# Performance work log

Hardware: AMD Instinct MI355X
Metric: run time of the kernel (lower is better)

The kernel has to match this reference:

```python
import jax, jax.numpy as jnp
import numpy as np

B, T, D, H = 512, 512, 256, 512

def setup_inputs() -> dict:
    key = jax.random.key(0)
    ks = jax.random.split(key, 7)
    s_ih = 1.0 / np.sqrt(H)
    return {
        "x": jax.random.normal(ks[0], (B, T, D), dtype=jnp.float32),
        "W_ih": jax.random.normal(ks[1], (4 * H, D), dtype=jnp.float32) * s_ih,
        "W_hh": jax.random.normal(ks[2], (4 * H, H), dtype=jnp.float32) * s_ih,
        "b_ih": jax.random.normal(ks[3], (4 * H,), dtype=jnp.float32) * s_ih,
        "b_hh": jax.random.normal(ks[4], (4 * H,), dtype=jnp.float32) * s_ih,
        "W_fc": jax.random.normal(ks[5], (1, H), dtype=jnp.float32) * s_ih,
        "b_fc": jax.random.normal(ks[6], (1,), dtype=jnp.float32) * s_ih,
    }

def reference(x, W_ih, W_hh, b_ih, b_hh, W_fc, b_fc):
    # Precompute input projections for all steps: [T, B, 4H]
    xg = jnp.einsum('btd,gd->tbg', x, W_ih) + b_ih + b_hh

    def step(carry, xg_t):
        h, c = carry
        gates = xg_t + h @ W_hh.T  # [B, 4H]
        i, f, g, o = jnp.split(gates, 4, axis=-1)  # torch LSTMCell gate order
        i = jax.nn.sigmoid(i)
        f = jax.nn.sigmoid(f)
        g = jnp.tanh(g)
        o = jax.nn.sigmoid(o)
        c = f * c + i * g
        h = o * jnp.tanh(c)
        return (h, c), None

    h0 = jnp.zeros((x.shape[0], W_hh.shape[1]), dtype=x.dtype)
    (h, _), _ = jax.lax.scan(step, (h0, h0), xg)
    # dropout in eval mode is identity
    return jax.nn.sigmoid(h @ W_fc.T + b_fc)  # [B, 1]
```

## Files before the change

### kernel.cpp

```cpp
#include <hip/hip_runtime.h>

typedef _Float16 f16;
typedef _Float16 f16x8 __attribute__((ext_vector_type(8)));
typedef float f32x4 __attribute__((ext_vector_type(4)));
typedef unsigned int u32;
typedef u32 u32x4 __attribute__((ext_vector_type(4)));
typedef unsigned long long u64;

#define TT 512
#define BB 512
#define DD 256
#define HH 512

#define WPACK_BYTES (32*4*24*64*8*2)
#define HBUF_OFF    (WPACK_BYTES)
#define HQ_SLOT     (BB*HH/4)
#define HBUF_BYTES  (4*BB*HH*2)

__device__ __forceinline__ float sigf(float v) {
    return __frcp_rn(1.0f + __expf(-v));
}
__device__ __forceinline__ float tanh_fast(float v) {
    float e = __expf(2.0f * fminf(v, 15.0f));
    return 1.0f - 2.0f * __frcp_rn(e + 1.0f);
}

__global__ void pack_w(const float* __restrict__ W_ih,
                       const float* __restrict__ W_hh,
                       f16* __restrict__ Wp) {
    int tid = blockIdx.x * 256 + threadIdx.x;
    if (tid >= 32*4*24*64) return;
    int lane = tid & 63;
    int rest = tid >> 6;
    int ks   = rest % 24;
    int t3   = rest / 24;
    int nt   = t3 & 3;
    int ji   = t3 >> 2;
    int g  = nt*512 + ji*16 + (lane & 15);
    int k0 = ks*32 + ((lane >> 4) & 3)*8;
    const float* src = (k0 < 256) ? (W_ih + (size_t)g*DD + k0)
                                  : (W_hh + (size_t)g*HH + (k0 - 256));
    f16x8 v;
    #pragma unroll
    for (int j = 0; j < 8; ++j) v[j] = (f16)src[j];
    *(f16x8*)(Wp + (size_t)tid*8) = v;
}

#define LDH16_SC1(A, p) asm volatile(                                  \
    "global_load_dwordx4 %0, %16, off sc1\n\t"                         \
    "global_load_dwordx4 %1, %16, off offset:64 sc1\n\t"               \
    "global_load_dwordx4 %2, %16, off offset:128 sc1\n\t"              \
    "global_load_dwordx4 %3, %16, off offset:192 sc1\n\t"              \
    "global_load_dwordx4 %4, %16, off offset:256 sc1\n\t"              \
    "global_load_dwordx4 %5, %16, off offset:320 sc1\n\t"              \
    "global_load_dwordx4 %6, %16, off offset:384 sc1\n\t"              \
    "global_load_dwordx4 %7, %16, off offset:448 sc1\n\t"              \
    "global_load_dwordx4 %8, %16, off offset:512 sc1\n\t"              \
    "global_load_dwordx4 %9, %16, off offset:576 sc1\n\t"              \
    "global_load_dwordx4 %10, %16, off offset:640 sc1\n\t"             \
    "global_load_dwordx4 %11, %16, off offset:704 sc1\n\t"             \
    "global_load_dwordx4 %12, %16, off offset:768 sc1\n\t"             \
    "global_load_dwordx4 %13, %16, off offset:832 sc1\n\t"             \
    "global_load_dwordx4 %14, %16, off offset:896 sc1\n\t"             \
    "global_load_dwordx4 %15, %16, off offset:960 sc1\n\t"             \
    "s_waitcnt vmcnt(0)"                                               \
    : "=&v"((A)[0]), "=&v"((A)[1]), "=&v"((A)[2]), "=&v"((A)[3]),      \
      "=&v"((A)[4]), "=&v"((A)[5]), "=&v"((A)[6]), "=&v"((A)[7]),      \
      "=&v"((A)[8]), "=&v"((A)[9]), "=&v"((A)[10]), "=&v"((A)[11]),    \
      "=&v"((A)[12]), "=&v"((A)[13]), "=&v"((A)[14]), "=&v"((A)[15])   \
    : "v"(p) : "memory")

#define LDH256_SC1(A, p) asm volatile(                                 \
    "global_load_dwordx4 %0, %16, off sc1\n\t"                         \
    "global_load_dwordx4 %1, %16, off offset:16 sc1\n\t"               \
    "global_load_dwordx4 %2, %16, off offset:32 sc1\n\t"               \
    "global_load_dwordx4 %3, %16, off offset:48 sc1\n\t"               \
    "global_load_dwordx4 %4, %16, off offset:64 sc1\n\t"               \
    "global_load_dwordx4 %5, %16, off offset:80 sc1\n\t"               \
    "global_load_dwordx4 %6, %16, off offset:96 sc1\n\t"               \
    "global_load_dwordx4 %7, %16, off offset:112 sc1\n\t"              \
    "global_load_dwordx4 %8, %16, off offset:128 sc1\n\t"              \
    "global_load_dwordx4 %9, %16, off offset:144 sc1\n\t"              \
    "global_load_dwordx4 %10, %16, off offset:160 sc1\n\t"             \
    "global_load_dwordx4 %11, %16, off offset:176 sc1\n\t"             \
    "global_load_dwordx4 %12, %16, off offset:192 sc1\n\t"             \
    "global_load_dwordx4 %13, %16, off offset:208 sc1\n\t"             \
    "global_load_dwordx4 %14, %16, off offset:224 sc1\n\t"             \
    "global_load_dwordx4 %15, %16, off offset:240 sc1\n\t"             \
    "s_waitcnt vmcnt(0)"                                               \
    : "=&v"((A)[0]), "=&v"((A)[1]), "=&v"((A)[2]), "=&v"((A)[3]),      \
      "=&v"((A)[4]), "=&v"((A)[5]), "=&v"((A)[6]), "=&v"((A)[7]),      \
      "=&v"((A)[8]), "=&v"((A)[9]), "=&v"((A)[10]), "=&v"((A)[11]),    \
      "=&v"((A)[12]), "=&v"((A)[13]), "=&v"((A)[14]), "=&v"((A)[15])   \
    : "v"(p) : "memory")

__device__ __forceinline__ bool chunk_ok(const f16x8& c) {
    u32x4 t = __builtin_bit_cast(u32x4, c);
    return ((t.y >> 16) != 0xFFFFu) && ((t.w >> 16) != 0xFFFFu);
}

__launch_bounds__(256, 1)
__global__ void lstm_fused(const float* __restrict__ x,
                           const float* __restrict__ b_ih,
                           const float* __restrict__ b_hh,
                           const float* __restrict__ W_fc,
                           const float* __restrict__ b_fc,
                           const f16* __restrict__ Wp,
                           f16* __restrict__ hbuf,
                           float* __restrict__ out) {
    extern __shared__ char smem[];
    f16x8* Wlds = (f16x8*)smem;

    const int tid  = threadIdx.x;
    const int lane = tid & 63;
    const int w    = tid >> 6;
    const int bi   = blockIdx.x & 7;
    const int ji   = blockIdx.x >> 3;

    {
        const f16x8* src = (const f16x8*)Wp + (size_t)ji * (4*24*64);
        for (int i = tid; i < 4*24*64; i += 256) Wlds[i] = src[i];
    }

    const int uq = (lane >> 4) * 4;
    float bias[4][4];
    #pragma unroll
    for (int nt = 0; nt < 4; ++nt)
        #pragma unroll
        for (int r = 0; r < 4; ++r)
            bias[nt][r] = b_ih[nt*512 + ji*16 + uq + r] + b_hh[nt*512 + ji*16 + uq + r];
    __syncthreads();

    const int batch  = bi*64 + w*16 + (lane & 15);
    const int koff   = (lane >> 4) * 8;
    const float* xrow = x + (size_t)batch * TT * DD + koff;
    u64* hq = (u64*)hbuf;
    const int hrow_q = (batch * HH + koff) >> 2;
    const int hoff_q = (batch * HH + ji*16 + uq) >> 2;

    float c[4] = {0.f, 0.f, 0.f, 0.f};
    f32x4 acc[4];

    {
        float4 xa[8], xb[8];
        #pragma unroll
        for (int ks = 0; ks < 8; ++ks) {
            xa[ks] = *(const float4*)(xrow + ks*32);
            xb[ks] = *(const float4*)(xrow + ks*32 + 4);
        }
        #pragma unroll
        for (int nt = 0; nt < 4; ++nt)
            acc[nt] = (f32x4){bias[nt][0], bias[nt][1], bias[nt][2], bias[nt][3]};
        #pragma unroll
        for (int ks = 0; ks < 8; ++ks) {
            f16x8 a;
            a[0]=(f16)xa[ks].x; a[1]=(f16)xa[ks].y; a[2]=(f16)xa[ks].z; a[3]=(f16)xa[ks].w;
            a[4]=(f16)xb[ks].x; a[5]=(f16)xb[ks].y; a[6]=(f16)xb[ks].z; a[7]=(f16)xb[ks].w;
            #pragma unroll
            for (int nt = 0; nt < 4; ++nt)
                acc[nt] = __builtin_amdgcn_mfma_f32_16x16x32_f16(
                    Wlds[(nt*24 + ks)*64 + lane], a, acc[nt], 0, 0, 0);
        }
    }

    for (int s = 0; s < TT; ++s) {
        if (s > 0) {
            const u64* hb = hq + (size_t)(s & 3) * HQ_SLOT + hrow_q;
            f16x8 Ah[16];
            for (;;) {
                LDH16_SC1(Ah, hb);
                bool ok = true;
                #pragma unroll
                for (int ks = 0; ks < 16; ++ks) ok = ok && chunk_ok(Ah[ks]);
                if (__all(ok)) break;
                __builtin_amdgcn_s_sleep(2);
            }
            if (s + 3 <= TT)
                __hip_atomic_store(hq + (size_t)((s + 3) & 3) * HQ_SLOT + hoff_q,
                                   0xFFFFFFFFFFFFFFFFull, __ATOMIC_RELAXED,
                                   __HIP_MEMORY_SCOPE_AGENT);
            #pragma unroll
            for (int ks = 0; ks < 16; ++ks)
                #pragma unroll
                for (int nt = 0; nt < 4; ++nt)
                    acc[nt] = __builtin_amdgcn_mfma_f32_16x16x32_f16(
                        Wlds[(nt*24 + ks + 8)*64 + lane], Ah[ks], acc[nt], 0, 0, 0);
        } else {
            __hip_atomic_store(hq + (size_t)3 * HQ_SLOT + hoff_q,
                               0xFFFFFFFFFFFFFFFFull, __ATOMIC_RELAXED,
                               __HIP_MEMORY_SCOPE_AGENT);
        }

        union { u64 q; f16 h4[4]; } H;
        #pragma unroll
        for (int r = 0; r < 4; ++r) {
            float ig = sigf(acc[0][r]);
            float fg = sigf(acc[1][r]);
            float gg = tanh_fast(acc[2][r]);
            float og = sigf(acc[3][r]);
            c[r] = fg * c[r] + ig * gg;
            H.h4[r] = (f16)(og * tanh_fast(c[r]));
        }

        asm volatile("s_waitcnt vmcnt(0)" ::: "memory");
        __hip_atomic_store(hq + (size_t)((s + 1) & 3) * HQ_SLOT + hoff_q, H.q,
                           __ATOMIC_RELAXED, __HIP_MEMORY_SCOPE_AGENT);

        if (s + 1 < TT) {
            const float* xs = xrow + (size_t)(s + 1) * DD;
            float4 na[8], nb[8];
            #pragma unroll
            for (int ks = 0; ks < 8; ++ks) {
                na[ks] = *(const float4*)(xs + ks*32);
                nb[ks] = *(const float4*)(xs + ks*32 + 4);
            }
            #pragma unroll
            for (int nt = 0; nt < 4; ++nt)
                acc[nt] = (f32x4){bias[nt][0], bias[nt][1], bias[nt][2], bias[nt][3]};
            #pragma unroll
            for (int ks = 0; ks < 8; ++ks) {
                f16x8 a;
                a[0]=(f16)na[ks].x; a[1]=(f16)na[ks].y; a[2]=(f16)na[ks].z; a[3]=(f16)na[ks].w;
                a[4]=(f16)nb[ks].x; a[5]=(f16)nb[ks].y; a[6]=(f16)nb[ks].z; a[7]=(f16)nb[ks].w;
                #pragma unroll
                for (int nt = 0; nt < 4; ++nt)
                    acc[nt] = __builtin_amdgcn_mfma_f32_16x16x32_f16(
                        Wlds[(nt*24 + ks)*64 + lane], a, acc[nt], 0, 0, 0);
            }
        }
    }

    if (ji == 0) {
        const u64* hr = hq + (size_t)(TT & 3) * HQ_SLOT
                      + (((size_t)(bi*64 + (tid >> 2)) * HH + (tid & 3)*128) >> 2);
        f16x8 Hh[16];
        for (;;) {
            LDH256_SC1(Hh, hr);
            bool ok = true;
            #pragma unroll
            for (int ks = 0; ks < 16; ++ks) ok = ok && chunk_ok(Hh[ks]);
            if (__all(ok)) break;
            __builtin_amdgcn_s_sleep(2);
        }
        const float* wf = W_fc + (tid & 3)*128;
        float ssum = 0.f;
        #pragma unroll
        for (int c2 = 0; c2 < 16; ++c2)
            #pragma unroll
            for (int e = 0; e < 8; ++e)
                ssum += (float)Hh[c2][e] * wf[c2*8 + e];
        __syncthreads();
        float* red = (float*)smem;
        red[(tid >> 2)*4 + (tid & 3)] = ssum;
        __syncthreads();
        if (tid < 64) {
            float v = red[tid*4+0] + red[tid*4+1] + red[tid*4+2] + red[tid*4+3] + b_fc[0];
            out[bi*64 + tid] = sigf(v);
        }
    }
}

extern "C" void kernel_launch(void* const* d_in, const int* in_sizes, int n_in,
                              void* d_out, int out_size, void* d_ws, size_t ws_size,
                              hipStream_t stream) {
    const float* x    = (const float*)d_in[0];
    const float* W_ih = (const float*)d_in[1];
    const float* W_hh = (const float*)d_in[2];
    const float* b_ih = (const float*)d_in[3];
    const float* b_hh = (const float*)d_in[4];
    const float* W_fc = (const float*)d_in[5];
    const float* b_fc = (const float*)d_in[6];
    float* out = (float*)d_out;

    f16* Wp   = (f16*)d_ws;
    f16* hbuf = (f16*)((char*)d_ws + HBUF_OFF);

    hipMemsetAsync(hbuf, 0xFF, HBUF_BYTES, stream);
    pack_w<<<768, 256, 0, stream>>>(W_ih, W_hh, Wp);

    static bool attr_set = []() {
        hipFuncSetAttribute(reinterpret_cast<const void*>(lstm_fused),
                            hipFuncAttributeMaxDynamicSharedMemorySize, 98304);
        return true;
    }();
    (void)attr_set;

    void* kargs[] = {(void*)&x, (void*)&b_ih, (void*)&b_hh, (void*)&W_fc,
                     (void*)&b_fc, (void*)&Wp, (void*)&hbuf, (void*)&out};
    hipError_t e = hipLaunchCooperativeKernel(
        reinterpret_cast<const void*>(lstm_fused),
        dim3(256), dim3(256), kargs, 98304, stream);
    if (e != hipSuccess) {
        lstm_fused<<<dim3(256), dim3(256), 98304, stream>>>(
            x, b_ih, b_hh, W_fc, b_fc, Wp, hbuf, out);
    }
}
```

Measured before the change: 2.620 ms.

## Prefetch next-step x into LDS asynchronously during the recurrent h wait

Issues global_load_lds DMA copies of the next timestep's x slice at the top of each step so the load overlaps the h spin-wait and recurrent MFMAs. The input projection then reads x from LDS instead of issuing global loads after the h store. This removes exposed global-load latency from the serial critical path. It raises dynamic LDS to 160 KB per block and relies on the vmcnt wait before the h store to cover completion of the async copies.

```diff
diff --git a/kernel.cpp b/kernel.cpp
--- a/kernel.cpp
+++ b/kernel.cpp
@@ -16,6 +16,9 @@
 #define HBUF_OFF    (WPACK_BYTES)
 #define HQ_SLOT     (BB*HH/4)
 #define HBUF_BYTES  (4*BB*HH*2)
+
+#define XLDS_OFF    98304
+#define LDS_TOTAL   163840
 
 __device__ __forceinline__ float sigf(float v) {
     return __frcp_rn(1.0f + __expf(-v));
@@ -99,6 +102,41 @@
     return ((t.y >> 16) != 0xFFFFu) && ((t.w >> 16) != 0xFFFFu);
 }
 
+typedef __attribute__((address_space(1))) const unsigned int as1_u32;
+typedef __attribute__((address_space(3))) unsigned int as3_u32;
+
+__device__ __forceinline__ void x_stage(const float* __restrict__ xsrc,
+                                        float* __restrict__ ldsx) {
+    #pragma unroll
+    for (int i = 0; i < 16; ++i) {
+        __builtin_amdgcn_global_load_lds(
+            (as1_u32*)(xsrc + (i >> 1)*32 + (i & 1)*4),
+            (as3_u32*)(ldsx + i*256), 16, 0, 0);
+    }
+}
+
+__device__ __forceinline__ void x_mfma_lds(f32x4 (&acc)[4],
+                                           const float* __restrict__ ldsx,
+                                           const f16x8* __restrict__ Wlds,
+                                           const float (&bias)[4][4], int lane) {
+    #pragma unroll
+    for (int nt = 0; nt < 4; ++nt)
+        acc[nt] = (f32x4){bias[nt][0], bias[nt][1], bias[nt][2], bias[nt][3]};
+    const float4* xs4 = (const float4*)ldsx;
+    #pragma unroll
+    for (int ks = 0; ks < 8; ++ks) {
+        float4 a0 = xs4[(2*ks)*64 + lane];
+        float4 a1 = xs4[(2*ks + 1)*64 + lane];
+        f16x8 a;
+        a[0]=(f16)a0.x; a[1]=(f16)a0.y; a[2]=(f16)a0.z; a[3]=(f16)a0.w;
+        a[4]=(f16)a1.x; a[5]=(f16)a1.y; a[6]=(f16)a1.z; a[7]=(f16)a1.w;
+        #pragma unroll
+        for (int nt = 0; nt < 4; ++nt)
+            acc[nt] = __builtin_amdgcn_mfma_f32_16x16x32_f16(
+                Wlds[(nt*24 + ks)*64 + lane], a, acc[nt], 0, 0, 0);
+    }
+}
+
 __launch_bounds__(256, 1)
 __global__ void lstm_fused(const float* __restrict__ x,
                            const float* __restrict__ b_ih,
@@ -116,6 +154,7 @@
     const int w    = tid >> 6;
     const int bi   = blockIdx.x & 7;
     const int ji   = blockIdx.x >> 3;
+    float* ldsx = (float*)(smem + XLDS_OFF) + w * 4096;
 
     {
         const f16x8* src = (const f16x8*)Wp + (size_t)ji * (4*24*64);
@@ -164,6 +203,8 @@
     }
 
     for (int s = 0; s < TT; ++s) {
+        if (s + 1 < TT) x_stage(xrow + (size_t)(s + 1) * DD, ldsx);
+
         if (s > 0) {
             const u64* hb = hq + (size_t)(s & 3) * HQ_SLOT + hrow_q;
             f16x8 Ah[16];
@@ -206,28 +247,7 @@
         __hip_atomic_store(hq + (size_t)((s + 1) & 3) * HQ_SLOT + hoff_q, H.q,
                            __ATOMIC_RELAXED, __HIP_MEMORY_SCOPE_AGENT);
 
-        if (s + 1 < TT) {
-            const float* xs = xrow + (size_t)(s + 1) * DD;
-            float4 na[8], nb[8];
-            #pragma unroll
-            for (int ks = 0; ks < 8; ++ks) {
-                na[ks] = *(const float4*)(xs + ks*32);
-                nb[ks] = *(const float4*)(xs + ks*32 + 4);
-            }
-            #pragma unroll
-            for (int nt = 0; nt < 4; ++nt)
-                acc[nt] = (f32x4){bias[nt][0], bias[nt][1], bias[nt][2], bias[nt][3]};
-            #pragma unroll
-            for (int ks = 0; ks < 8; ++ks) {
-                f16x8 a;
-                a[0]=(f16)na[ks].x; a[1]=(f16)na[ks].y; a[2]=(f16)na[ks].z; a[3]=(f16)na[ks].w;
-                a[4]=(f16)nb[ks].x; a[5]=(f16)nb[ks].y; a[6]=(f16)nb[ks].z; a[7]=(f16)nb[ks].w;
-                #pragma unroll
-                for (int nt = 0; nt < 4; ++nt)
-                    acc[nt] = __builtin_amdgcn_mfma_f32_16x16x32_f16(
-                        Wlds[(nt*24 + ks)*64 + lane], a, acc[nt], 0, 0, 0);
-            }
-        }
+        if (s + 1 < TT) x_mfma_lds(acc, ldsx, Wlds, bias, lane);
     }
 
     if (ji == 0) {
@@ -280,7 +300,7 @@
 
     static bool attr_set = []() {
         hipFuncSetAttribute(reinterpret_cast<const void*>(lstm_fused),
-                            hipFuncAttributeMaxDynamicSharedMemorySize, 98304);
+                            hipFuncAttributeMaxDynamicSharedMemorySize, LDS_TOTAL);
         return true;
     }();
     (void)attr_set;
@@ -289,9 +309,9 @@
                      (void*)&b_fc, (void*)&Wp, (void*)&hbuf, (void*)&out};
     hipError_t e = hipLaunchCooperativeKernel(
         reinterpret_cast<const void*>(lstm_fused),
-        dim3(256), dim3(256), kargs, 98304, stream);
+        dim3(256), dim3(256), kargs, LDS_TOTAL, stream);
     if (e != hipSuccess) {
-        lstm_fused<<<dim3(256), dim3(256), 98304, stream>>>(
+        lstm_fused<<<dim3(256), dim3(256), LDS_TOTAL, stream>>>(
             x, b_ih, b_hh, W_fc, b_fc, Wp, hbuf, out);
     }
 }
```

Measured after the change: 3.838 ms. +46.5%, slower.

## Process two batch groups per block to overlap recurrent step latency

Applied to the files above, without the earlier changes.

Halves the grid to 128 blocks and gives each block two independent batch groups, A and B, which run in alternating steps. While one group waits on its hidden-state spin-poll, the other group's gate math and input projection can proceed. This is meant to hide the cross-block synchronisation latency. In exchange, each block does twice the work per step, uses more registers, and half the CUs go idle.

```diff
diff --git a/kernel.cpp b/kernel.cpp
--- a/kernel.cpp
+++ b/kernel.cpp
@@ -99,6 +99,83 @@
     return ((t.y >> 16) != 0xFFFFu) && ((t.w >> 16) != 0xFFFFu);
 }
 
+__device__ __forceinline__ void x_tail(
+    int snext, f32x4 (&acc)[4], const float* __restrict__ xrow,
+    const f16x8* __restrict__ Wlds, const float (&bias)[4][4], int lane)
+{
+    const float* xs = xrow + (size_t)snext * DD;
+    float4 na[8], nb[8];
+    #pragma unroll
+    for (int ks = 0; ks < 8; ++ks) {
+        na[ks] = *(const float4*)(xs + ks*32);
+        nb[ks] = *(const float4*)(xs + ks*32 + 4);
+    }
+    #pragma unroll
+    for (int nt = 0; nt < 4; ++nt)
+        acc[nt] = (f32x4){bias[nt][0], bias[nt][1], bias[nt][2], bias[nt][3]};
+    #pragma unroll
+    for (int ks = 0; ks < 8; ++ks) {
+        f16x8 a;
+        a[0]=(f16)na[ks].x; a[1]=(f16)na[ks].y; a[2]=(f16)na[ks].z; a[3]=(f16)na[ks].w;
+        a[4]=(f16)nb[ks].x; a[5]=(f16)nb[ks].y; a[6]=(f16)nb[ks].z; a[7]=(f16)nb[ks].w;
+        #pragma unroll
+        for (int nt = 0; nt < 4; ++nt)
+            acc[nt] = __builtin_amdgcn_mfma_f32_16x16x32_f16(
+                Wlds[(nt*24 + ks)*64 + lane], a, acc[nt], 0, 0, 0);
+    }
+}
+
+__device__ __forceinline__ void step_pipe(
+    int s, f32x4 (&acc)[4], float (&c)[4],
+    const f16x8* __restrict__ Wlds, u64* __restrict__ hq,
+    int hrow_q, int hoff_q, const float* __restrict__ xrow,
+    const float (&bias)[4][4], int lane)
+{
+    if (s > 0) {
+        const u64* hb = hq + (size_t)(s & 3) * HQ_SLOT + hrow_q;
+        f16x8 Ah[16];
+        for (;;) {
+            LDH16_SC1(Ah, hb);
+            bool ok = true;
+            #pragma unroll
+            for (int ks = 0; ks < 16; ++ks) ok = ok && chunk_ok(Ah[ks]);
+            if (__all(ok)) break;
+            __builtin_amdgcn_s_sleep(2);
+        }
+        if (s + 3 <= TT)
+            __hip_atomic_store(hq + (size_t)((s + 3) & 3) * HQ_SLOT + hoff_q,
+                               0xFFFFFFFFFFFFFFFFull, __ATOMIC_RELAXED,
+                               __HIP_MEMORY_SCOPE_AGENT);
+        #pragma unroll
+        for (int ks = 0; ks < 16; ++ks)
+            #pragma unroll
+            for (int nt = 0; nt < 4; ++nt)
+                acc[nt] = __builtin_amdgcn_mfma_f32_16x16x32_f16(
+                    Wlds[(nt*24 + ks + 8)*64 + lane], Ah[ks], acc[nt], 0, 0, 0);
+    } else {
+        __hip_atomic_store(hq + (size_t)3 * HQ_SLOT + hoff_q,
+                           0xFFFFFFFFFFFFFFFFull, __ATOMIC_RELAXED,
+                           __HIP_MEMORY_SCOPE_AGENT);
+    }
+
+    union { u64 q; f16 h4[4]; } H;
+    #pragma unroll
+    for (int r = 0; r < 4; ++r) {
+        float ig = sigf(acc[0][r]);
+        float fg = sigf(acc[1][r]);
+        float gg = tanh_fast(acc[2][r]);
+        float og = sigf(acc[3][r]);
+        c[r] = fg * c[r] + ig * gg;
+        H.h4[r] = (f16)(og * tanh_fast(c[r]));
+    }
+
+    asm volatile("s_waitcnt vmcnt(0)" ::: "memory");
+    __hip_atomic_store(hq + (size_t)((s + 1) & 3) * HQ_SLOT + hoff_q, H.q,
+                       __ATOMIC_RELAXED, __HIP_MEMORY_SCOPE_AGENT);
+
+    if (s + 1 < TT) x_tail(s + 1, acc, xrow, Wlds, bias, lane);
+}
+
 __launch_bounds__(256, 1)
 __global__ void lstm_fused(const float* __restrict__ x,
                            const float* __restrict__ b_ih,
@@ -114,8 +191,10 @@
     const int tid  = threadIdx.x;
     const int lane = tid & 63;
     const int w    = tid >> 6;
-    const int bi   = blockIdx.x & 7;
-    const int ji   = blockIdx.x >> 3;
+    const int ji   = blockIdx.x & 31;
+    const int p    = blockIdx.x >> 5;
+    const int gA   = p;
+    const int gB   = p + 4;
 
     {
         const f16x8* src = (const f16x8*)Wp + (size_t)ji * (4*24*64);
@@ -131,131 +210,62 @@
             bias[nt][r] = b_ih[nt*512 + ji*16 + uq + r] + b_hh[nt*512 + ji*16 + uq + r];
     __syncthreads();
 
-    const int batch  = bi*64 + w*16 + (lane & 15);
-    const int koff   = (lane >> 4) * 8;
-    const float* xrow = x + (size_t)batch * TT * DD + koff;
+    const int koff = (lane >> 4) * 8;
     u64* hq = (u64*)hbuf;
-    const int hrow_q = (batch * HH + koff) >> 2;
-    const int hoff_q = (batch * HH + ji*16 + uq) >> 2;
-
-    float c[4] = {0.f, 0.f, 0.f, 0.f};
-    f32x4 acc[4];
-
-    {
-        float4 xa[8], xb[8];
-        #pragma unroll
-        for (int ks = 0; ks < 8; ++ks) {
-            xa[ks] = *(const float4*)(xrow + ks*32);
-            xb[ks] = *(const float4*)(xrow + ks*32 + 4);
-        }
-        #pragma unroll
-        for (int nt = 0; nt < 4; ++nt)
-            acc[nt] = (f32x4){bias[nt][0], bias[nt][1], bias[nt][2], bias[nt][3]};
-        #pragma unroll
-        for (int ks = 0; ks < 8; ++ks) {
-            f16x8 a;
-            a[0]=(f16)xa[ks].x; a[1]=(f16)xa[ks].y; a[2]=(f16)xa[ks].z; a[3]=(f16)xa[ks].w;
-            a[4]=(f16)xb[ks].x; a[5]=(f16)xb[ks].y; a[6]=(f16)xb[ks].z; a[7]=(f16)xb[ks].w;
-            #pragma unroll
-            for (int nt = 0; nt < 4; ++nt)
-                acc[nt] = __builtin_amdgcn_mfma_f32_16x16x32_f16(
-                    Wlds[(nt*24 + ks)*64 + lane], a, acc[nt], 0, 0, 0);
-        }
-    }
+
+    const int batchA = gA*64 + w*16 + (lane & 15);
+    const int batchB = gB*64 + w*16 + (lane & 15);
+    const float* xrowA = x + (size_t)batchA * TT * DD + koff;
+    const float* xrowB = x + (size_t)batchB * TT * DD + koff;
+    const int hrowA = (batchA * HH + koff) >> 2;
+    const int hrowB = (batchB * HH + koff) >> 2;
+    const int hoffA = (batchA * HH + ji*16 + uq) >> 2;
+    const int hoffB = (batchB * HH + ji*16 + uq) >> 2;
+
+    float cA[4] = {0.f, 0.f, 0.f, 0.f};
+    float cB[4] = {0.f, 0.f, 0.f, 0.f};
+    f32x4 accA[4], accB[4];
+
+    x_tail(0, accA, xrowA, Wlds, bias, lane);
+    x_tail(0, accB, xrowB, Wlds, bias, lane);
 
     for (int s = 0; s < TT; ++s) {
-        if (s > 0) {
-            const u64* hb = hq + (size_t)(s & 3) * HQ_SLOT + hrow_q;
-            f16x8 Ah[16];
+        step_pipe(s, accA, cA, Wlds, hq, hrowA, hoffA, xrowA, bias, lane);
+        step_pipe(s, accB, cB, Wlds, hq, hrowB, hoffB, xrowB, bias, lane);
+    }
+
+    if (ji == 0) {
+        #pragma unroll 1
+        for (int gi = 0; gi < 2; ++gi) {
+            const int g = (gi == 0) ? gA : gB;
+            const u64* hr = hq + (size_t)(TT & 3) * HQ_SLOT
+                          + (((size_t)(g*64 + (tid >> 2)) * HH + (tid & 3)*128) >> 2);
+            f16x8 Hh[16];
             for (;;) {
-                LDH16_SC1(Ah, hb);
+                LDH256_SC1(Hh, hr);
                 bool ok = true;
                 #pragma unroll
-                for (int ks = 0; ks < 16; ++ks) ok = ok && chunk_ok(Ah[ks]);
+                for (int ks = 0; ks < 16; ++ks) ok = ok && chunk_ok(Hh[ks]);
                 if (__all(ok)) break;
                 __builtin_amdgcn_s_sleep(2);
             }
-            if (s + 3 <= TT)
-                __hip_atomic_store(hq + (size_t)((s + 3) & 3) * HQ_SLOT + hoff_q,
-                                   0xFFFFFFFFFFFFFFFFull, __ATOMIC_RELAXED,
-                                   __HIP_MEMORY_SCOPE_AGENT);
+            const float* wf = W_fc + (tid & 3)*128;
+            float ssum = 0.f;
             #pragma unroll
-            for (int ks = 0; ks < 16; ++ks)
+            for (int c2 = 0; c2 < 16; ++c2)
                 #pragma unroll
-                for (int nt = 0; nt < 4; ++nt)
-                    acc[nt] = __builtin_amdgcn_mfma_f32_16x16x32_f16(
-                        Wlds[(nt*24 + ks + 8)*64 + lane], Ah[ks], acc[nt], 0, 0, 0);
-        } else {
-            __hip_atomic_store(hq + (size_t)3 * HQ_SLOT + hoff_q,
-                               0xFFFFFFFFFFFFFFFFull, __ATOMIC_RELAXED,
-                               __HIP_MEMORY_SCOPE_AGENT);
-        }
-
-        union { u64 q; f16 h4[4]; } H;
-        #pragma unroll
-        for (int r = 0; r < 4; ++r) {
-            float ig = sigf(acc[0][r]);
-            float fg = sigf(acc[1][r]);
-            float gg = tanh_fast(acc[2][r]);
-            float og = sigf(acc[3][r]);
-            c[r] = fg * c[r] + ig * gg;
-            H.h4[r] = (f16)(og * tanh_fast(c[r]));
-        }
-
-        asm volatile("s_waitcnt vmcnt(0)" ::: "memory");
-        __hip_atomic_store(hq + (size_t)((s + 1) & 3) * HQ_SLOT + hoff_q, H.q,
-                           __ATOMIC_RELAXED, __HIP_MEMORY_SCOPE_AGENT);
-
-        if (s + 1 < TT) {
-            const float* xs = xrow + (size_t)(s + 1) * DD;
-            float4 na[8], nb[8];
-            #pragma unroll
-            for (int ks = 0; ks < 8; ++ks) {
-                na[ks] = *(const float4*)(xs + ks*32);
-                nb[ks] = *(const float4*)(xs + ks*32 + 4);
+                for (int e = 0; e < 8; ++e)
+                    ssum += (float)Hh[c2][e] * wf[c2*8 + e];
+            __syncthreads();
+            float* red = (float*)smem;
+            red[(tid >> 2)*4 + (tid & 3)] = ssum;
+            __syncthreads();
+            if (tid < 64) {
+                float v = red[tid*4+0] + red[tid*4+1] + red[tid*4+2] + red[tid*4+3]
+                        + b_fc[0];
+                out[g*64 + tid] = sigf(v);
             }
-            #pragma unroll
-            for (int nt = 0; nt < 4; ++nt)
-                acc[nt] = (f32x4){bias[nt][0], bias[nt][1], bias[nt][2], bias[nt][3]};
-            #pragma unroll
-            for (int ks = 0; ks < 8; ++ks) {
-                f16x8 a;
-                a[0]=(f16)na[ks].x; a[1]=(f16)na[ks].y; a[2]=(f16)na[ks].z; a[3]=(f16)na[ks].w;
-                a[4]=(f16)nb[ks].x; a[5]=(f16)nb[ks].y; a[6]=(f16)nb[ks].z; a[7]=(f16)nb[ks].w;
-                #pragma unroll
-                for (int nt = 0; nt < 4; ++nt)
-                    acc[nt] = __builtin_amdgcn_mfma_f32_16x16x32_f16(
-                        Wlds[(nt*24 + ks)*64 + lane], a, acc[nt], 0, 0, 0);
-            }
-        }
-    }
-
-    if (ji == 0) {
-        const u64* hr = hq + (size_t)(TT & 3) * HQ_SLOT
-                      + (((size_t)(bi*64 + (tid >> 2)) * HH + (tid & 3)*128) >> 2);
-        f16x8 Hh[16];
-        for (;;) {
-            LDH256_SC1(Hh, hr);
-            bool ok = true;
-            #pragma unroll
-            for (int ks = 0; ks < 16; ++ks) ok = ok && chunk_ok(Hh[ks]);
-            if (__all(ok)) break;
-            __builtin_amdgcn_s_sleep(2);
-        }
-        const float* wf = W_fc + (tid & 3)*128;
-        float ssum = 0.f;
-        #pragma unroll
-        for (int c2 = 0; c2 < 16; ++c2)
-            #pragma unroll
-            for (int e = 0; e < 8; ++e)
-                ssum += (float)Hh[c2][e] * wf[c2*8 + e];
-        __syncthreads();
-        float* red = (float*)smem;
-        red[(tid >> 2)*4 + (tid & 3)] = ssum;
-        __syncthreads();
-        if (tid < 64) {
-            float v = red[tid*4+0] + red[tid*4+1] + red[tid*4+2] + red[tid*4+3] + b_fc[0];
-            out[bi*64 + tid] = sigf(v);
+            __syncthreads();
         }
     }
 }
@@ -289,9 +299,9 @@
                      (void*)&b_fc, (void*)&Wp, (void*)&hbuf, (void*)&out};
     hipError_t e = hipLaunchCooperativeKernel(
         reinterpret_cast<const void*>(lstm_fused),
-        dim3(256), dim3(256), kargs, 98304, stream);
+        dim3(128), dim3(256), kargs, 98304, stream);
     if (e != hipSuccess) {
-        lstm_fused<<<dim3(256), dim3(256), 98304, stream>>>(
+        lstm_fused<<<dim3(128), dim3(256), 98304, stream>>>(
             x, b_ih, b_hh, W_fc, b_fc, Wp, hbuf, out);
     }
 }
```

New measurement: 4.960 ms. 1.89x slower.
